# Performance work log

Hardware: AMD Instinct MI355X
Metric: run time of the kernel (lower is better)

The kernel has to match this reference:

```python
import jax, jax.numpy as jnp
import numpy as np

H = 1024; B = 8; L = 4096
DI = 2048   # d_inner = expand*H
DS = 16     # d_state
DC = 4      # d_conv
DR = 64     # dt_rank = ceil(H/16)
HR = 256    # H // 4 hourglass


def setup_inputs() -> dict:
    key = jax.random.key(0)
    ks = jax.random.split(key, 16)
    w = lambda k, s, sc=0.02: jax.random.normal(k, s, jnp.float32) * sc
    return {
        "x": jax.random.normal(ks[0], (B, L, H), jnp.float32),
        "c": jax.random.normal(ks[1], (B, H), jnp.float32),
        "adaln_w": w(ks[2], (3 * H, H)), "adaln_b": jnp.zeros((3 * H,), jnp.float32),
        "hgd_w1": w(ks[3], (HR, H)), "hgd_b1": jnp.zeros((HR,), jnp.float32),
        "hgd_w2": w(ks[4], (H, HR)), "hgd_b2": jnp.zeros((H,), jnp.float32),
        "hgf_wm": w(ks[5], (HR, H)), "hgf_bm": jnp.zeros((HR,), jnp.float32),
        "hgf_wr": w(ks[6], (HR, H)), "hgf_br": jnp.zeros((HR,), jnp.float32),
        "hgf_wf": w(ks[7], (H, HR)), "hgf_bf": jnp.zeros((H,), jnp.float32),
        "in_w": w(ks[8], (2 * DI, H)),
        "conv_w": w(ks[9], (DI, DC), 0.1), "conv_b": jnp.zeros((DI,), jnp.float32),
        "xproj_w": w(ks[10], (DR + 2 * DS, DI)),
        "dtproj_w": w(ks[11], (DI, DR), 0.1),
        "dt_bias": jnp.full((DI,), -4.6, jnp.float32),  # softplus -> dt ~ 0.01
        "A_log": jnp.log(jnp.tile(jnp.arange(1, DS + 1, dtype=jnp.float32), (DI, 1))),
        "D": jnp.ones((DI,), jnp.float32),
        "out_w": w(ks[12], (H, DI)),
    }


def reference(x, c, adaln_w, adaln_b, hgd_w1, hgd_b1, hgd_w2, hgd_b2,
              hgf_wm, hgf_bm, hgf_wr, hgf_br, hgf_wf, hgf_bf,
              in_w, conv_w, conv_b, xproj_w, dtproj_w, dt_bias, A_log, D, out_w):
    silu = jax.nn.silu
    # adaLN-Zero conditioning: SiLU -> Linear -> 3 chunks
    mod = silu(c) @ adaln_w.T + adaln_b                      # [B, 3H]
    shift, scale, alpha = jnp.split(mod, 3, axis=1)          # each [B, H]
    # LayerNorm (no affine, eps=1e-6)
    mu = x.mean(-1, keepdims=True)
    var = x.var(-1, keepdims=True)
    xn = (x - mu) / jnp.sqrt(var + 1e-6)
    x1 = xn * (1.0 + scale[:, None, :]) + shift[:, None, :]  # modulate
    # Hourglass dense: Linear(H->H/4) -> SiLU -> Linear(H/4->H)
    hd = silu(x1 @ hgd_w1.T + hgd_b1) @ hgd_w2.T + hgd_b2    # [B, L, H]
    # ---- Mamba ----
    xz = hd @ in_w.T                                         # [B, L, 2*DI]
    xm, z = jnp.split(xz, 2, axis=-1)
    # causal depthwise conv1d
    xc = jnp.transpose(xm, (0, 2, 1))                        # [B, DI, L]
    xc = jax.lax.conv_general_dilated(
        xc, conv_w[:, None, :], (1,), [(DC - 1, 0)],
        feature_group_count=DI, dimension_numbers=("NCH", "OIH", "NCH"))
    xc = silu(xc + conv_b[None, :, None])
    xc = jnp.transpose(xc, (0, 2, 1))                        # [B, L, DI]
    # input-dependent dt, B, C
    dbl = xc @ xproj_w.T                                     # [B, L, DR+2*DS]
    dt, Bm, Cm = jnp.split(dbl, [DR, DR + DS], axis=-1)
    dt = jax.nn.softplus(dt @ dtproj_w.T + dt_bias)          # [B, L, DI]
    A = -jnp.exp(A_log)                                      # [DI, DS]
    # selective scan: h_{t} = exp(dt*A)*h_{t-1} + dt*B_t*x_t ; y_t = <h_t, C_t>
    def step(h, inp):
        dt_t, B_t, C_t, x_t = inp                            # [B,DI],[B,DS],[B,DS],[B,DI]
        h = h * jnp.exp(dt_t[:, :, None] * A) + (dt_t * x_t)[:, :, None] * B_t[:, None, :]
        return h, jnp.einsum("bds,bs->bd", h, C_t)
    h0 = jnp.zeros((x.shape[0], DI, DS), x.dtype)
    seq = (jnp.transpose(dt, (1, 0, 2)), jnp.transpose(Bm, (1, 0, 2)),
           jnp.transpose(Cm, (1, 0, 2)), jnp.transpose(xc, (1, 0, 2)))
    _, ys = jax.lax.scan(step, h0, seq)                      # [L, B, DI]
    y = jnp.transpose(ys, (1, 0, 2)) + xc * D
    y = y * silu(z)
    x1_2 = y @ out_w.T                                       # [B, L, H]
    # Hourglass fusion
    fused = (silu(x1_2 @ hgf_wm.T + hgf_bm) * silu(x1 @ hgf_wr.T + hgf_br)) @ hgf_wf.T + hgf_bf
    return x + alpha[:, None, :] * fused
```

## Files before the change

### kernel.cpp

```cpp
#include <hip/hip_runtime.h>

#define Hn 1024
#define Bn 8
#define Ln 4096
#define DIn 2048
#define NCH 64
#define CLn 64

typedef __attribute__((ext_vector_type(8))) short short8;
typedef __attribute__((ext_vector_type(4))) short short4v;
typedef __attribute__((ext_vector_type(4))) float f32x4;

__device__ __forceinline__ float bf2f(short s) {
  return __uint_as_float(((unsigned)(unsigned short)s) << 16);
}
__device__ __forceinline__ short f2bf(float f) {
  unsigned u = __float_as_uint(f);
  u += 0x7fffu + ((u >> 16) & 1u);
  return (short)(u >> 16);
}
__device__ __forceinline__ float silu_f(float x) { return x / (1.f + __expf(-x)); }
__device__ __forceinline__ float softplus_f(float x) { return x > 20.f ? x : log1pf(__expf(x)); }

__device__ __forceinline__ void gld16(const short* g, short* l) {
  __builtin_amdgcn_global_load_lds((const __attribute__((address_space(1))) void*)g,
                                   (__attribute__((address_space(3))) void*)l, 16, 0, 0);
}

__global__ __launch_bounds__(256) void f2bf4_kernel(const float* __restrict__ in,
                                                    short* __restrict__ out, int n4) {
  int i = blockIdx.x * 256 + threadIdx.x;
  if (i < n4) {
    f32x4 v = ((const f32x4*)in)[i];
    short4v o;
    o.x = f2bf(v.x); o.y = f2bf(v.y); o.z = f2bf(v.z); o.w = f2bf(v.w);
    ((short4v*)out)[i] = o;
  }
}

__global__ __launch_bounds__(256) void modcalc_kernel(const float* __restrict__ c,
    const float* __restrict__ aw, const float* __restrict__ ab, float* __restrict__ mod) {
  int wid = blockIdx.x * 4 + (threadIdx.x >> 6);
  int lane = threadIdx.x & 63;
  int b = wid / 3072, n = wid - b * 3072;
  const f32x4* cr = (const f32x4*)(c + b * Hn);
  const f32x4* wr = (const f32x4*)(aw + (size_t)n * Hn);
  float s = 0.f;
#pragma unroll
  for (int i = 0; i < 4; ++i) {
    f32x4 cv = cr[lane + 64 * i];
    f32x4 wv = wr[lane + 64 * i];
    s += silu_f(cv.x) * wv.x + silu_f(cv.y) * wv.y + silu_f(cv.z) * wv.z + silu_f(cv.w) * wv.w;
  }
#pragma unroll
  for (int m = 1; m < 64; m <<= 1) s += __shfl_xor(s, m, 64);
  if (lane == 0) mod[wid] = s + ab[n];
}

__global__ __launch_bounds__(256) void ln_mod_kernel(const float* __restrict__ x,
    const float* __restrict__ mod, short* __restrict__ x1, int b0) {
  int row = blockIdx.x * 4 + (threadIdx.x >> 6);
  int lane = threadIdx.x & 63;
  int b = b0 + (row >> 12);
  const f32x4* xr = (const f32x4*)(x + (size_t)row * Hn);
  f32x4 v[4];
  float s = 0.f, ss = 0.f;
#pragma unroll
  for (int i = 0; i < 4; ++i) {
    v[i] = xr[lane + 64 * i];
    s += v[i].x + v[i].y + v[i].z + v[i].w;
    ss += v[i].x * v[i].x + v[i].y * v[i].y + v[i].z * v[i].z + v[i].w * v[i].w;
  }
#pragma unroll
  for (int m = 1; m < 64; m <<= 1) {
    s += __shfl_xor(s, m, 64);
    ss += __shfl_xor(ss, m, 64);
  }
  float mu = s * (1.f / 1024.f);
  float var = ss * (1.f / 1024.f) - mu * mu;
  float r = rsqrtf(var + 1e-6f);
  const f32x4* shp = (const f32x4*)(mod + b * 3072);
  const f32x4* scp = (const f32x4*)(mod + b * 3072 + 1024);
#pragma unroll
  for (int i = 0; i < 4; ++i) {
    int k4 = lane + 64 * i;
    f32x4 sc = scp[k4], sh = shp[k4];
    short4v o;
    o.x = f2bf((v[i].x - mu) * r * (1.f + sc.x) + sh.x);
    o.y = f2bf((v[i].y - mu) * r * (1.f + sc.y) + sh.y);
    o.z = f2bf((v[i].z - mu) * r * (1.f + sc.z) + sh.z);
    o.w = f2bf((v[i].w - mu) * r * (1.f + sc.w) + sh.w);
    *(short4v*)&x1[(size_t)row * Hn + k4 * 4] = o;
  }
}

#define SA_STR 40
template <int EPI>
__global__ __launch_bounds__(256) void gemm_k(
    const short* __restrict__ A, const short* __restrict__ W,
    const float* __restrict__ bias, const short* mul,
    const float* __restrict__ xres, const float* __restrict__ modp,
    void* outp, int N, int K, int b0) {
  __shared__ short sA[2][128 * SA_STR];
  __shared__ short sB[2][128 * SA_STR];
  int tid = threadIdx.x;
  int wave = tid >> 6, lane = tid & 63;
  int bm0 = blockIdx.y * 128;
  int bn0 = blockIdx.x * 128;
  int wm = (wave >> 1) * 64, wn = (wave & 1) * 64;
  int lrow = lane & 15, kh = (lane >> 4) * 8;
  int srow = tid >> 2;
  int scol = (tid & 3) * 8;

  f32x4 acc[4][4];
#pragma unroll
  for (int i = 0; i < 4; i++)
#pragma unroll
    for (int j = 0; j < 4; j++) acc[i][j] = (f32x4)0.f;

#pragma unroll
  for (int p = 0; p < 2; ++p) {
    int r = srow + p * 64;
    short8 av = *(const short8*)&A[(size_t)(bm0 + r) * K + scol];
    *(short8*)&sA[0][r * SA_STR + scol] = av;
    int n = bn0 + r;
    short8 bv = (short8)0;
    if (n < N) bv = *(const short8*)&W[(size_t)n * K + scol];
    *(short8*)&sB[0][r * SA_STR + scol] = bv;
  }
  __syncthreads();

  int cur = 0;
  for (int k0 = 0; k0 < K; k0 += 32) {
    bool have = (k0 + 32) < K;
    short8 av[2], bv[2];
    if (have) {
#pragma unroll
      for (int p = 0; p < 2; ++p) {
        int r = srow + p * 64;
        av[p] = *(const short8*)&A[(size_t)(bm0 + r) * K + k0 + 32 + scol];
        int n = bn0 + r;
        bv[p] = (short8)0;
        if (n < N) bv[p] = *(const short8*)&W[(size_t)n * K + k0 + 32 + scol];
      }
    }
    short8 af[4], bfr[4];
#pragma unroll
    for (int i = 0; i < 4; i++) af[i] = *(const short8*)&sA[cur][(wm + i * 16 + lrow) * SA_STR + kh];
#pragma unroll
    for (int j = 0; j < 4; j++) bfr[j] = *(const short8*)&sB[cur][(wn + j * 16 + lrow) * SA_STR + kh];
#pragma unroll
    for (int i = 0; i < 4; i++)
#pragma unroll
      for (int j = 0; j < 4; j++)
        acc[i][j] = __builtin_amdgcn_mfma_f32_16x16x32_bf16(af[i], bfr[j], acc[i][j], 0, 0, 0);
    if (have) {
      int nxt = cur ^ 1;
#pragma unroll
      for (int p = 0; p < 2; ++p) {
        int r = srow + p * 64;
        *(short8*)&sA[nxt][r * SA_STR + scol] = av[p];
        *(short8*)&sB[nxt][r * SA_STR + scol] = bv[p];
      }
    }
    __syncthreads();
    cur ^= 1;
  }

  int orow4 = (lane >> 4) * 4;
  int ocol = lane & 15;
#pragma unroll
  for (int i = 0; i < 4; i++)
#pragma unroll
    for (int j = 0; j < 4; j++)
#pragma unroll
      for (int r = 0; r < 4; r++) {
        int row = bm0 + wm + i * 16 + orow4 + r;
        int col = bn0 + wn + j * 16 + ocol;
        if (col >= N) continue;
        float v = acc[i][j][r];
        size_t idx = (size_t)row * N + col;
        if (EPI == 0) {
          ((short*)outp)[idx] = f2bf(v);
        } else if (EPI == 1) {
          ((short*)outp)[idx] = f2bf(v + bias[col]);
        } else if (EPI == 2) {
          ((short*)outp)[idx] = f2bf(silu_f(v + bias[col]));
        } else if (EPI == 3) {
          ((short*)outp)[idx] = f2bf(softplus_f(v + bias[col]));
        } else if (EPI == 4) {
          float t = silu_f(v + bias[col]) * bf2f(mul[idx]);
          ((short*)outp)[idx] = f2bf(t);
        } else if (EPI == 5) {
          ((float*)outp)[idx] = v;
        } else if (EPI == 6) {
          int b = b0 + (row >> 12);
          float t = v + bias[col];
          ((float*)outp)[idx] = xres[idx] + modp[b * 3072 + 2048 + col] * t;
        } else if (EPI == 7) {
          float t = silu_f(v) * bf2f(mul[idx]);
          ((short*)outp)[idx] = f2bf(t);
        }
      }
}

template <int EPI>
__global__ __launch_bounds__(256) void gemm_lds_k(
    const short* __restrict__ A, const short* __restrict__ W,
    const short* mul, void* outp, int N, int K) {
  __shared__ short sA[2][128 * 32];
  __shared__ short sB[2][128 * 32];
  int tid = threadIdx.x;
  int wave = tid >> 6, lane = tid & 63;
  int nwg = gridDim.x * gridDim.y;
  int orig = blockIdx.y * gridDim.x + blockIdx.x;
  int cpx = nwg >> 3;
  int wg = (orig & 7) * cpx + (orig >> 3);
  int bm0 = (wg / gridDim.x) * 128;
  int bn0 = (wg % gridDim.x) * 128;
  int wm = (wave >> 1) * 64, wn = (wave & 1) * 64;
  int lrow = lane & 15, kh = (lane >> 4) * 8;
  int srow = tid >> 2;
  int scol = (tid & 3) * 8;
  int soff = srow * 32 + scol;

  const short* Ab = A + (size_t)(bm0 + srow) * K + scol;
  const short* Bb = W + (size_t)(bn0 + srow) * K + scol;

  f32x4 acc[4][4];
#pragma unroll
  for (int i = 0; i < 4; i++)
#pragma unroll
    for (int j = 0; j < 4; j++) acc[i][j] = (f32x4)0.f;

  gld16(Ab, &sA[0][soff]);
  gld16(Ab + (size_t)64 * K, &sA[0][soff + 64 * 32]);
  gld16(Bb, &sB[0][soff]);
  gld16(Bb + (size_t)64 * K, &sB[0][soff + 64 * 32]);
  __syncthreads();

  int cur = 0;
  for (int k0 = 0; k0 < K; k0 += 32) {
    int nxt = cur ^ 1;
    if (k0 + 32 < K) {
      gld16(Ab + k0 + 32, &sA[nxt][soff]);
      gld16(Ab + k0 + 32 + (size_t)64 * K, &sA[nxt][soff + 64 * 32]);
      gld16(Bb + k0 + 32, &sB[nxt][soff]);
      gld16(Bb + k0 + 32 + (size_t)64 * K, &sB[nxt][soff + 64 * 32]);
    }
    short8 af[4], bfr[4];
#pragma unroll
    for (int i = 0; i < 4; i++) af[i] = *(const short8*)&sA[cur][(wm + i * 16 + lrow) * 32 + kh];
#pragma unroll
    for (int j = 0; j < 4; j++) bfr[j] = *(const short8*)&sB[cur][(wn + j * 16 + lrow) * 32 + kh];
#pragma unroll
    for (int i = 0; i < 4; i++)
#pragma unroll
      for (int j = 0; j < 4; j++)
        acc[i][j] = __builtin_amdgcn_mfma_f32_16x16x32_bf16(af[i], bfr[j], acc[i][j], 0, 0, 0);
    __syncthreads();
    cur = nxt;
  }

  int orow4 = (lane >> 4) * 4;
  int ocol = lane & 15;
#pragma unroll
  for (int i = 0; i < 4; i++)
#pragma unroll
    for (int j = 0; j < 4; j++)
#pragma unroll
      for (int r = 0; r < 4; r++) {
        int row = bm0 + wm + i * 16 + orow4 + r;
        int col = bn0 + wn + j * 16 + ocol;
        float v = acc[i][j][r];
        size_t idx = (size_t)row * N + col;
        if (EPI == 0) {
          ((short*)outp)[idx] = f2bf(v);
        } else if (EPI == 7) {
          float t = silu_f(v) * bf2f(mul[idx]);
          ((short*)outp)[idx] = f2bf(t);
        }
      }
}

__global__ __launch_bounds__(256) void conv_kernel(const short* __restrict__ xm,
    const float* __restrict__ cw, const float* __restrict__ cb, short* __restrict__ xc) {
  size_t idx = (size_t)blockIdx.x * 256 + threadIdx.x;
  int d = (int)(idx & (DIn - 1));
  size_t bt = idx >> 11;
  int t = (int)(bt & (Ln - 1));
  f32x4 w = *(const f32x4*)(cw + d * 4);
  float wj[4] = {w.x, w.y, w.z, w.w};
  float acc = cb[d];
#pragma unroll
  for (int j = 0; j < 4; ++j) {
    int tt = t - 3 + j;
    if (tt >= 0) acc += bf2f(xm[(bt - 3 + j) * DIn + d]) * wj[j];
  }
  xc[idx] = f2bf(silu_f(acc));
}

__global__ __launch_bounds__(256) void dtslice_kernel(const float* __restrict__ dbl,
                                                      short* __restrict__ dtb) {
  int idx = blockIdx.x * 256 + threadIdx.x;
  int row = idx >> 6, col = idx & 63;
  dtb[idx] = f2bf(dbl[(size_t)row * 96 + col]);
}

__global__ __launch_bounds__(256) void scan_part1(const short* __restrict__ dt,
    const short* __restrict__ xc, const float* __restrict__ dbl,
    const float* __restrict__ A_log, float* __restrict__ hq, float* __restrict__ sd) {
  __shared__ float sB[CLn * 16];
  int tid = threadIdx.x;
  int g = blockIdx.x * 256 + tid;
  int d = g & (DIn - 1);
  int r = g >> 11;
  int c = r & (NCH - 1);
  int b = r >> 6;
  size_t rb = (size_t)b * Ln + (size_t)c * CLn;
  {
    int row = tid >> 2, q = tid & 3;
    *(f32x4*)&sB[row * 16 + q * 4] = *(const f32x4*)(dbl + (rb + row) * 96 + 64 + q * 4);
  }
  __syncthreads();
  float A[16], h[16];
#pragma unroll
  for (int s = 0; s < 16; ++s) {
    A[s] = -__expf(A_log[d * 16 + s]);
    h[s] = 0.f;
  }
  bool st = true;
#pragma unroll
  for (int s = 1; s < 16; ++s)
    st = st && (fabsf(A[s] - (float)(s + 1) * A[0]) <= 1e-4f * fabsf(A[s]));
  float A0 = A[0];
  float sum = 0.f;
  const short* dp = dt + rb * DIn + d;
  const short* xp = xc + rb * DIn + d;
  short dtn = *dp, xcn = *xp;
  if (st) {
    for (int t = 0; t < CLn; ++t) {
      float dtv = bf2f(dtn), xv = bf2f(xcn);
      int tn = (t + 1 < CLn) ? t + 1 : t;
      dtn = dp[(size_t)tn * DIn];
      xcn = xp[(size_t)tn * DIn];
      float u = dtv * xv;
      sum += dtv;
      const f32x4* bp = (const f32x4*)&sB[t * 16];
      f32x4 b0 = bp[0], b1 = bp[1], b2 = bp[2], b3 = bp[3];
      float bv[16] = {b0.x, b0.y, b0.z, b0.w, b1.x, b1.y, b1.z, b1.w,
                      b2.x, b2.y, b2.z, b2.w, b3.x, b3.y, b3.z, b3.w};
      float qe = __expf(dtv * A0);
      float pk = qe;
#pragma unroll
      for (int s = 0; s < 16; ++s) {
        h[s] = h[s] * pk + u * bv[s];
        pk *= qe;
      }
    }
  } else {
    for (int t = 0; t < CLn; ++t) {
      float dtv = bf2f(dtn), xv = bf2f(xcn);
      int tn = (t + 1 < CLn) ? t + 1 : t;
      dtn = dp[(size_t)tn * DIn];
      xcn = xp[(size_t)tn * DIn];
      float u = dtv * xv;
      sum += dtv;
      const f32x4* bp = (const f32x4*)&sB[t * 16];
      f32x4 b0 = bp[0], b1 = bp[1], b2 = bp[2], b3 = bp[3];
      float bv[16] = {b0.x, b0.y, b0.z, b0.w, b1.x, b1.y, b1.z, b1.w,
                      b2.x, b2.y, b2.z, b2.w, b3.x, b3.y, b3.z, b3.w};
#pragma unroll
      for (int s = 0; s < 16; ++s) h[s] = h[s] * __expf(dtv * A[s]) + u * bv[s];
    }
  }
  size_t bd = (size_t)b * DIn + d;
  f32x4* out = (f32x4*)(hq + (bd * NCH + c) * 16);
#pragma unroll
  for (int i = 0; i < 4; ++i) {
    f32x4 o; o.x = h[4 * i]; o.y = h[4 * i + 1]; o.z = h[4 * i + 2]; o.w = h[4 * i + 3];
    out[i] = o;
  }
  sd[bd * NCH + c] = sum;
}

__global__ __launch_bounds__(256) void scan_combine(const float* __restrict__ A_log,
    const float* __restrict__ sd, float* hq) {
  int g = blockIdx.x * 256 + threadIdx.x;
  int s = g & 15;
  size_t bd = (size_t)(g >> 4);
  int d = (int)(bd & (DIn - 1));
  float A = -__expf(A_log[d * 16 + s]);
  float H = 0.f;
  for (int c = 0; c < NCH; ++c) {
    size_t idx = (bd * NCH + c) * 16 + s;
    float he = hq[idx];
    float e = __expf(A * sd[bd * NCH + c]);
    hq[idx] = H;
    H = H * e + he;
  }
}

__global__ __launch_bounds__(256) void scan_part2(const short* dt,
    const short* __restrict__ xc, const float* __restrict__ dbl,
    const float* __restrict__ A_log, const float* __restrict__ Dv,
    const float* __restrict__ hq, short* y) {
  __shared__ float sBC[CLn * 32];
  int tid = threadIdx.x;
  int g = blockIdx.x * 256 + tid;
  int d = g & (DIn - 1);
  int r = g >> 11;
  int c = r & (NCH - 1);
  int b = r >> 6;
  size_t rb = (size_t)b * Ln + (size_t)c * CLn;
  {
    int row = tid >> 2, q = tid & 3;
    const float* src = dbl + (rb + row) * 96 + 64 + q * 8;
    *(f32x4*)&sBC[row * 32 + q * 8] = *(const f32x4*)src;
    *(f32x4*)&sBC[row * 32 + q * 8 + 4] = *(const f32x4*)(src + 4);
  }
  __syncthreads();
  size_t bd = (size_t)b * DIn + d;
  float A[16], h[16];
#pragma unroll
  for (int s = 0; s < 16; ++s) A[s] = -__expf(A_log[d * 16 + s]);
  const f32x4* hin = (const f32x4*)(hq + (bd * NCH + c) * 16);
#pragma unroll
  for (int i = 0; i < 4; ++i) {
    f32x4 qv = hin[i];
    h[4 * i] = qv.x; h[4 * i + 1] = qv.y; h[4 * i + 2] = qv.z; h[4 * i + 3] = qv.w;
  }
  bool st = true;
#pragma unroll
  for (int s = 1; s < 16; ++s)
    st = st && (fabsf(A[s] - (float)(s + 1) * A[0]) <= 1e-4f * fabsf(A[s]));
  float A0 = A[0];
  float Dd = Dv[d];
  const short* dp = dt + rb * DIn + d;
  const short* xp = xc + rb * DIn + d;
  short* yp = y + rb * DIn + d;
  short dtn = *dp, xcn = *xp;
  if (st) {
    for (int t = 0; t < CLn; ++t) {
      float dtv = bf2f(dtn), xv = bf2f(xcn);
      int tn = (t + 1 < CLn) ? t + 1 : t;
      dtn = dp[(size_t)tn * DIn];
      xcn = xp[(size_t)tn * DIn];
      float u = dtv * xv;
      const f32x4* pp = (const f32x4*)&sBC[t * 32];
      f32x4 v0 = pp[0], v1 = pp[1], v2 = pp[2], v3 = pp[3];
      f32x4 v4 = pp[4], v5 = pp[5], v6 = pp[6], v7 = pp[7];
      float bc[32] = {v0.x, v0.y, v0.z, v0.w, v1.x, v1.y, v1.z, v1.w,
                      v2.x, v2.y, v2.z, v2.w, v3.x, v3.y, v3.z, v3.w,
                      v4.x, v4.y, v4.z, v4.w, v5.x, v5.y, v5.z, v5.w,
                      v6.x, v6.y, v6.z, v6.w, v7.x, v7.y, v7.z, v7.w};
      float qe = __expf(dtv * A0);
      float pk = qe, acc = 0.f;
#pragma unroll
      for (int s = 0; s < 16; ++s) {
        h[s] = h[s] * pk + u * bc[s];
        acc += h[s] * bc[16 + s];
        pk *= qe;
      }
      yp[(size_t)t * DIn] = f2bf(acc + xv * Dd);
    }
  } else {
    for (int t = 0; t < CLn; ++t) {
      float dtv = bf2f(dtn), xv = bf2f(xcn);
      int tn = (t + 1 < CLn) ? t + 1 : t;
      dtn = dp[(size_t)tn * DIn];
      xcn = xp[(size_t)tn * DIn];
      float u = dtv * xv;
      const f32x4* pp = (const f32x4*)&sBC[t * 32];
      f32x4 v0 = pp[0], v1 = pp[1], v2 = pp[2], v3 = pp[3];
      f32x4 v4 = pp[4], v5 = pp[5], v6 = pp[6], v7 = pp[7];
      float bc[32] = {v0.x, v0.y, v0.z, v0.w, v1.x, v1.y, v1.z, v1.w,
                      v2.x, v2.y, v2.z, v2.w, v3.x, v3.y, v3.z, v3.w,
                      v4.x, v4.y, v4.z, v4.w, v5.x, v5.y, v5.z, v5.w,
                      v6.x, v6.y, v6.z, v6.w, v7.x, v7.y, v7.z, v7.w};
      float acc = 0.f;
#pragma unroll
      for (int s = 0; s < 16; ++s) {
        h[s] = h[s] * __expf(dtv * A[s]) + u * bc[s];
        acc += h[s] * bc[16 + s];
      }
      yp[(size_t)t * DIn] = f2bf(acc + xv * Dd);
    }
  }
}

extern "C" void kernel_launch(void* const* d_in, const int* in_sizes, int n_in,
                              void* d_out, int out_size, void* d_ws, size_t ws_size,
                              hipStream_t stream) {
  const float* x = (const float*)d_in[0];
  const float* c = (const float*)d_in[1];
  const float* adaln_w = (const float*)d_in[2];
  const float* adaln_b = (const float*)d_in[3];
  const float* hgd_w1 = (const float*)d_in[4];
  const float* hgd_b1 = (const float*)d_in[5];
  const float* hgd_w2 = (const float*)d_in[6];
  const float* hgd_b2 = (const float*)d_in[7];
  const float* hgf_wm = (const float*)d_in[8];
  const float* hgf_bm = (const float*)d_in[9];
  const float* hgf_wr = (const float*)d_in[10];
  const float* hgf_br = (const float*)d_in[11];
  const float* hgf_wf = (const float*)d_in[12];
  const float* hgf_bf = (const float*)d_in[13];
  const float* in_w = (const float*)d_in[14];
  const float* conv_w = (const float*)d_in[15];
  const float* conv_b = (const float*)d_in[16];
  const float* xproj_w = (const float*)d_in[17];
  const float* dtproj_w = (const float*)d_in[18];
  const float* dt_bias = (const float*)d_in[19];
  const float* A_log = (const float*)d_in[20];
  const float* Dv = (const float*)d_in[21];
  const float* out_w = (const float*)d_in[22];
  (void)in_sizes; (void)n_in; (void)out_size;

  char* ws = (char*)d_ws;
  size_t off = 0;
  auto alloc = [&](size_t bytes) -> void* {
    void* p = ws + off;
    off += (bytes + 255) & ~(size_t)255;
    return p;
  };
  short* w1b = (short*)alloc((size_t)256 * 1024 * 2);
  short* w2b = (short*)alloc((size_t)1024 * 256 * 2);
  short* wmb = (short*)alloc((size_t)256 * 1024 * 2);
  short* wrb = (short*)alloc((size_t)256 * 1024 * 2);
  short* wfb = (short*)alloc((size_t)1024 * 256 * 2);
  short* inwb = (short*)alloc((size_t)4096 * 1024 * 2);
  short* xpb = (short*)alloc((size_t)96 * 2048 * 2);
  short* dtpb = (short*)alloc((size_t)2048 * 64 * 2);
  short* owb = (short*)alloc((size_t)1024 * 2048 * 2);
  float* modb = (float*)alloc((size_t)Bn * 3072 * 4);
  size_t persist = off;

  int BC = 8;
  while (BC > 1 && persist + (size_t)BC * Ln * 14976 > ws_size) BC >>= 1;
  int nchunk = 8 / BC;
  size_t Mc = (size_t)BC * Ln;

  short* x1 = (short*)alloc(Mc * 1024 * 2);
  short* hd = (short*)alloc(Mc * 1024 * 2);
  short* xm = (short*)alloc(Mc * 2048 * 2);
  short* xct = (short*)alloc(Mc * 2048 * 2);
  float* dbl = (float*)alloc(Mc * 96 * 4);
  short* dtb = (short*)alloc(Mc * 64 * 2);
  float* hq = (float*)alloc((size_t)BC * DIn * NCH * 16 * 4);
  float* sd = (float*)alloc((size_t)BC * DIn * NCH * 4);
  short* t1 = xct;

  auto conv1 = [&](const float* src, short* dst, int n) {
    f2bf4_kernel<<<(n / 4 + 255) / 256, 256, 0, stream>>>(src, dst, n / 4);
  };
  conv1(hgd_w1, w1b, 256 * 1024);
  conv1(hgd_w2, w2b, 1024 * 256);
  conv1(hgf_wm, wmb, 256 * 1024);
  conv1(hgf_wr, wrb, 256 * 1024);
  conv1(hgf_wf, wfb, 1024 * 256);
  conv1(in_w, inwb, 4096 * 1024);
  conv1(xproj_w, xpb, 96 * 2048);
  conv1(dtproj_w, dtpb, 2048 * 64);
  conv1(out_w, owb, 1024 * 2048);

  modcalc_kernel<<<(Bn * 3072) / 4, 256, 0, stream>>>(c, adaln_w, adaln_b, modb);

  dim3 blk(256);
  int gy = (int)(Mc / 128);
  for (int ck = 0; ck < nchunk; ++ck) {
    int b0 = ck * BC;
    const float* xch = x + (size_t)b0 * Ln * Hn;
    float* och = (float*)d_out + (size_t)b0 * Ln * Hn;

    ln_mod_kernel<<<(int)(Mc / 4), blk, 0, stream>>>(xch, modb, x1, b0);
    gemm_k<2><<<dim3(2, gy), blk, 0, stream>>>(x1, w1b, hgd_b1, nullptr, nullptr, nullptr, t1, 256, 1024, 0);
    gemm_k<1><<<dim3(8, gy), blk, 0, stream>>>(t1, w2b, hgd_b2, nullptr, nullptr, nullptr, hd, 1024, 256, 0);
    gemm_lds_k<0><<<dim3(16, gy), blk, 0, stream>>>(hd, inwb, nullptr, xm, 2048, 1024);
    conv_kernel<<<(int)(Mc * 2048 / 256), blk, 0, stream>>>(xm, conv_w, conv_b, xct);
    gemm_k<5><<<dim3(1, gy), blk, 0, stream>>>(xct, xpb, nullptr, nullptr, nullptr, nullptr, dbl, 96, 2048, 0);
    dtslice_kernel<<<(int)(Mc * 64 / 256), blk, 0, stream>>>(dbl, dtb);
    gemm_k<3><<<dim3(16, gy), blk, 0, stream>>>(dtb, dtpb, dt_bias, nullptr, nullptr, nullptr, xm, 2048, 64, 0);
    scan_part1<<<(int)(BC * 512), blk, 0, stream>>>(xm, xct, dbl, A_log, hq, sd);
    scan_combine<<<(int)(BC * 128), blk, 0, stream>>>(A_log, sd, hq);
    scan_part2<<<(int)(BC * 512), blk, 0, stream>>>(xm, xct, dbl, A_log, Dv, hq, xm);
    gemm_lds_k<7><<<dim3(16, gy), blk, 0, stream>>>(hd, inwb + (size_t)2048 * 1024, xm, xm, 2048, 1024);
    gemm_lds_k<0><<<dim3(8, gy), blk, 0, stream>>>(xm, owb, nullptr, hd, 1024, 2048);
    gemm_k<2><<<dim3(2, gy), blk, 0, stream>>>(hd, wmb, hgf_bm, nullptr, nullptr, nullptr, t1, 256, 1024, 0);
    gemm_k<4><<<dim3(2, gy), blk, 0, stream>>>(x1, wrb, hgf_br, t1, nullptr, nullptr, t1, 256, 1024, 0);
    gemm_k<6><<<dim3(8, gy), blk, 0, stream>>>(t1, wfb, hgf_bf, nullptr, xch, modb, och, 1024, 256, b0);
  }
}
```

Baseline: 2.033 ms.

## Use 256x256x64 tiled GEMM for large projections and fuse dt slice into xproj epilogue

Measured after the change: 2.091 ms. +2.8%, slower.

```diff
diff --git a/kernel.cpp b/kernel.cpp
--- a/kernel.cpp
+++ b/kernel.cpp
@@ -200,64 +200,75 @@
         } else if (EPI == 7) {
           float t = silu_f(v) * bf2f(mul[idx]);
           ((short*)outp)[idx] = f2bf(t);
+        } else if (EPI == 8) {
+          ((float*)outp)[idx] = v;
+          if (col < 64) ((short*)mul)[(size_t)row * 64 + col] = f2bf(v);
         }
       }
 }
 
 template <int EPI>
-__global__ __launch_bounds__(256) void gemm_lds_k(
+__global__ __launch_bounds__(512, 1) void gemm256_k(
     const short* __restrict__ A, const short* __restrict__ W,
     const short* mul, void* outp, int N, int K) {
-  __shared__ short sA[2][128 * 32];
-  __shared__ short sB[2][128 * 32];
+  __shared__ short sA[2][256 * 64];
+  __shared__ short sB[2][256 * 64];
   int tid = threadIdx.x;
   int wave = tid >> 6, lane = tid & 63;
   int nwg = gridDim.x * gridDim.y;
   int orig = blockIdx.y * gridDim.x + blockIdx.x;
   int cpx = nwg >> 3;
   int wg = (orig & 7) * cpx + (orig >> 3);
-  int bm0 = (wg / gridDim.x) * 128;
-  int bn0 = (wg % gridDim.x) * 128;
-  int wm = (wave >> 1) * 64, wn = (wave & 1) * 64;
-  int lrow = lane & 15, kh = (lane >> 4) * 8;
-  int srow = tid >> 2;
-  int scol = (tid & 3) * 8;
-  int soff = srow * 32 + scol;
+  int bm0 = (wg / gridDim.x) * 256;
+  int bn0 = (wg % gridDim.x) * 256;
+  int wm = (wave >> 2) * 128, wn = (wave & 3) * 64;
+  int lrow = lane & 15;
+  int kq = (lane >> 4) * 8;
+  int srow = tid >> 3;
+  int scol = (tid & 7) * 8;
+  int soff = srow * 64 + scol;
 
   const short* Ab = A + (size_t)(bm0 + srow) * K + scol;
   const short* Bb = W + (size_t)(bn0 + srow) * K + scol;
 
-  f32x4 acc[4][4];
-#pragma unroll
-  for (int i = 0; i < 4; i++)
-#pragma unroll
-    for (int j = 0; j < 4; j++) acc[i][j] = (f32x4)0.f;
-
-  gld16(Ab, &sA[0][soff]);
-  gld16(Ab + (size_t)64 * K, &sA[0][soff + 64 * 32]);
-  gld16(Bb, &sB[0][soff]);
-  gld16(Bb + (size_t)64 * K, &sB[0][soff + 64 * 32]);
+  f32x4 acc[8][4];
+#pragma unroll
+  for (int m = 0; m < 8; m++)
+#pragma unroll
+    for (int n = 0; n < 4; n++) acc[m][n] = (f32x4)0.f;
+
+#pragma unroll
+  for (int p = 0; p < 4; ++p) {
+    gld16(Ab + (size_t)(64 * p) * K, &sA[0][soff + p * 64 * 64]);
+    gld16(Bb + (size_t)(64 * p) * K, &sB[0][soff + p * 64 * 64]);
+  }
   __syncthreads();
 
   int cur = 0;
-  for (int k0 = 0; k0 < K; k0 += 32) {
+  for (int k0 = 0; k0 < K; k0 += 64) {
     int nxt = cur ^ 1;
-    if (k0 + 32 < K) {
-      gld16(Ab + k0 + 32, &sA[nxt][soff]);
-      gld16(Ab + k0 + 32 + (size_t)64 * K, &sA[nxt][soff + 64 * 32]);
-      gld16(Bb + k0 + 32, &sB[nxt][soff]);
-      gld16(Bb + k0 + 32 + (size_t)64 * K, &sB[nxt][soff + 64 * 32]);
-    }
-    short8 af[4], bfr[4];
-#pragma unroll
-    for (int i = 0; i < 4; i++) af[i] = *(const short8*)&sA[cur][(wm + i * 16 + lrow) * 32 + kh];
-#pragma unroll
-    for (int j = 0; j < 4; j++) bfr[j] = *(const short8*)&sB[cur][(wn + j * 16 + lrow) * 32 + kh];
-#pragma unroll
-    for (int i = 0; i < 4; i++)
-#pragma unroll
-      for (int j = 0; j < 4; j++)
-        acc[i][j] = __builtin_amdgcn_mfma_f32_16x16x32_bf16(af[i], bfr[j], acc[i][j], 0, 0, 0);
+    if (k0 + 64 < K) {
+#pragma unroll
+      for (int p = 0; p < 4; ++p) {
+        gld16(Ab + k0 + 64 + (size_t)(64 * p) * K, &sA[nxt][soff + p * 64 * 64]);
+        gld16(Bb + k0 + 64 + (size_t)(64 * p) * K, &sB[nxt][soff + p * 64 * 64]);
+      }
+    }
+#pragma unroll
+    for (int ks = 0; ks < 2; ++ks) {
+      short8 af[8], bfr[4];
+#pragma unroll
+      for (int m = 0; m < 8; ++m)
+        af[m] = *(const short8*)&sA[cur][(wm + m * 16 + lrow) * 64 + ks * 32 + kq];
+#pragma unroll
+      for (int n = 0; n < 4; ++n)
+        bfr[n] = *(const short8*)&sB[cur][(wn + n * 16 + lrow) * 64 + ks * 32 + kq];
+#pragma unroll
+      for (int m = 0; m < 8; ++m)
+#pragma unroll
+        for (int n = 0; n < 4; ++n)
+          acc[m][n] = __builtin_amdgcn_mfma_f32_16x16x32_bf16(af[m], bfr[n], acc[m][n], 0, 0, 0);
+    }
     __syncthreads();
     cur = nxt;
   }
@@ -265,14 +276,14 @@
   int orow4 = (lane >> 4) * 4;
   int ocol = lane & 15;
 #pragma unroll
-  for (int i = 0; i < 4; i++)
-#pragma unroll
-    for (int j = 0; j < 4; j++)
+  for (int m = 0; m < 8; m++)
+#pragma unroll
+    for (int n = 0; n < 4; n++)
 #pragma unroll
       for (int r = 0; r < 4; r++) {
-        int row = bm0 + wm + i * 16 + orow4 + r;
-        int col = bn0 + wn + j * 16 + ocol;
-        float v = acc[i][j][r];
+        int row = bm0 + wm + m * 16 + orow4 + r;
+        int col = bn0 + wn + n * 16 + ocol;
+        float v = acc[m][n][r];
         size_t idx = (size_t)row * N + col;
         if (EPI == 0) {
           ((short*)outp)[idx] = f2bf(v);
@@ -298,13 +309,6 @@
     if (tt >= 0) acc += bf2f(xm[(bt - 3 + j) * DIn + d]) * wj[j];
   }
   xc[idx] = f2bf(silu_f(acc));
-}
-
-__global__ __launch_bounds__(256) void dtslice_kernel(const float* __restrict__ dbl,
-                                                      short* __restrict__ dtb) {
-  int idx = blockIdx.x * 256 + threadIdx.x;
-  int row = idx >> 6, col = idx & 63;
-  dtb[idx] = f2bf(dbl[(size_t)row * 96 + col]);
 }
 
 __global__ __launch_bounds__(256) void scan_part1(const short* __restrict__ dt,
@@ -567,7 +571,9 @@
   modcalc_kernel<<<(Bn * 3072) / 4, 256, 0, stream>>>(c, adaln_w, adaln_b, modb);
 
   dim3 blk(256);
+  dim3 blk512(512);
   int gy = (int)(Mc / 128);
+  int gy256 = (int)(Mc / 256);
   for (int ck = 0; ck < nchunk; ++ck) {
     int b0 = ck * BC;
     const float* xch = x + (size_t)b0 * Ln * Hn;
@@ -576,16 +582,15 @@
     ln_mod_kernel<<<(int)(Mc / 4), blk, 0, stream>>>(xch, modb, x1, b0);
     gemm_k<2><<<dim3(2, gy), blk, 0, stream>>>(x1, w1b, hgd_b1, nullptr, nullptr, nullptr, t1, 256, 1024, 0);
     gemm_k<1><<<dim3(8, gy), blk, 0, stream>>>(t1, w2b, hgd_b2, nullptr, nullptr, nullptr, hd, 1024, 256, 0);
-    gemm_lds_k<0><<<dim3(16, gy), blk, 0, stream>>>(hd, inwb, nullptr, xm, 2048, 1024);
+    gemm256_k<0><<<dim3(8, gy256), blk512, 0, stream>>>(hd, inwb, nullptr, xm, 2048, 1024);
     conv_kernel<<<(int)(Mc * 2048 / 256), blk, 0, stream>>>(xm, conv_w, conv_b, xct);
-    gemm_k<5><<<dim3(1, gy), blk, 0, stream>>>(xct, xpb, nullptr, nullptr, nullptr, nullptr, dbl, 96, 2048, 0);
-    dtslice_kernel<<<(int)(Mc * 64 / 256), blk, 0, stream>>>(dbl, dtb);
+    gemm_k<8><<<dim3(1, gy), blk, 0, stream>>>(xct, xpb, nullptr, dtb, nullptr, nullptr, dbl, 96, 2048, 0);
     gemm_k<3><<<dim3(16, gy), blk, 0, stream>>>(dtb, dtpb, dt_bias, nullptr, nullptr, nullptr, xm, 2048, 64, 0);
     scan_part1<<<(int)(BC * 512), blk, 0, stream>>>(xm, xct, dbl, A_log, hq, sd);
     scan_combine<<<(int)(BC * 128), blk, 0, stream>>>(A_log, sd, hq);
     scan_part2<<<(int)(BC * 512), blk, 0, stream>>>(xm, xct, dbl, A_log, Dv, hq, xm);
-    gemm_lds_k<7><<<dim3(16, gy), blk, 0, stream>>>(hd, inwb + (size_t)2048 * 1024, xm, xm, 2048, 1024);
-    gemm_lds_k<0><<<dim3(8, gy), blk, 0, stream>>>(xm, owb, nullptr, hd, 1024, 2048);
+    gemm256_k<7><<<dim3(8, gy256), blk512, 0, stream>>>(hd, inwb + (size_t)2048 * 1024, xm, xm, 2048, 1024);
+    gemm256_k<0><<<dim3(4, gy256), blk512, 0, stream>>>(xm, owb, nullptr, hd, 1024, 2048);
     gemm_k<2><<<dim3(2, gy), blk, 0, stream>>>(hd, wmb, hgf_bm, nullptr, nullptr, nullptr, t1, 256, 1024, 0);
     gemm_k<4><<<dim3(2, gy), blk, 0, stream>>>(x1, wrb, hgf_br, t1, nullptr, nullptr, t1, 256, 1024, 0);
     gemm_k<6><<<dim3(8, gy), blk, 0, stream>>>(t1, wfb, hgf_bf, nullptr, xch, modb, och, 1024, 256, b0);
```
